# Performance work log

Measured on AMD Instinct MI355X. Metric: run time of the kernel, lower is better.

Reference implementation:

```python
import jax, jax.numpy as jnp
import numpy as np

TOP_K = 2


def setup_inputs() -> dict:
    key = jax.random.key(0)
    k1, k2, k3, k4, k5 = jax.random.split(key, 5)
    B, S, H, F, E = 4, 2048, 1024, 4096, 8
    scale = 1.0 / np.sqrt(H)
    return {
        "hidden_states": jax.random.normal(k1, (B, S, H), dtype=jnp.float32),
        "gate_w": jax.random.normal(k2, (E, H), dtype=jnp.float32) * scale,
        "w1": jax.random.normal(k3, (E, F, H), dtype=jnp.float32) * scale,
        "w3": jax.random.normal(k4, (E, F, H), dtype=jnp.float32) * scale,
        "w2": jax.random.normal(k5, (E, H, F), dtype=jnp.float32) * (1.0 / np.sqrt(F)),
    }


def reference(hidden_states, gate_w, w1, w3, w2):
    B, S, H = hidden_states.shape
    E = gate_w.shape[0]
    x = hidden_states.reshape(-1, H)                    # [T, H], T = B*S

    router_logits = x @ gate_w.T                        # [T, E]
    probs = jax.nn.softmax(router_logits.astype(jnp.float32), axis=-1)
    top_w, top_i = jax.lax.top_k(probs, TOP_K)          # [T, k]
    top_w = top_w / jnp.sum(top_w, axis=-1, keepdims=True)
    top_w = top_w.astype(x.dtype)

    # combine weight of each expert for each token: [E, T]
    one_hot = jax.nn.one_hot(top_i, E, dtype=x.dtype)   # [T, k, E]
    comb = jnp.einsum("tke,tk->et", one_hot, top_w)

    # loop over experts via scan; tokens not routed to expert e have comb==0,
    # which matches the gather/FFN/scatter-combine of the original exactly.
    def body(acc, wts):
        w1e, w3e, w2e, ce = wts
        h = jax.nn.silu(x @ w1e.T) * (x @ w3e.T)        # [T, F]
        return acc + (h @ w2e.T) * ce[:, None], None

    out0 = jnp.zeros_like(x)
    out, _ = jax.lax.scan(body, out0, (w1, w3, w2, comb))
    return out.reshape(B, S, H), router_logits
```

## Files before the change

kernel.cpp:

```cpp
#include <hip/hip_runtime.h>
#include <hip/hip_bf16.h>

#define T_TOK 8192
#define HDIM  1024
#define FDIM  4096
#define NEXP  8

typedef __attribute__((ext_vector_type(8))) short short8;
typedef __attribute__((ext_vector_type(4))) float f32x4;
typedef unsigned short u16;
typedef unsigned int   u32;

#define XB_OFF    0ull
#define W1B_OFF   (XB_OFF   + 16777216ull)
#define W3B_OFF   (W1B_OFF  + 67108864ull)
#define W2B_OFF   (W3B_OFF  + 67108864ull)
#define HBUF_OFF  (W2B_OFF  + 67108864ull)
#define CNT_OFF   (HBUF_OFF + 134217728ull)
#define HOFF_OFF  (CNT_OFF  + 64ull)
#define TLIST_OFF (HOFF_OFF + 64ull)
#define WLIST_OFF (TLIST_OFF + 262144ull)
#define WS_NEED   (WLIST_OFF + 262144ull)

__device__ __forceinline__ u16 f2bf(float f) {
  u32 u = __float_as_uint(f);
  return (u16)((u + 0x7fffu + ((u >> 16) & 1u)) >> 16);
}

__device__ __forceinline__ void gl_lds16(const void* g, void* l) {
  __builtin_amdgcn_global_load_lds(
      (const __attribute__((address_space(1))) void*)g,
      (__attribute__((address_space(3))) void*)l, 16, 0, 0);
}

__global__ __launch_bounds__(256) void prep_kernel(
    const float* __restrict__ x, const float* __restrict__ gw,
    const float* __restrict__ s0, const float* __restrict__ s1, const float* __restrict__ s2,
    u16* __restrict__ d0, u16* __restrict__ d1, u16* __restrict__ d2,
    float* __restrict__ logits, u16* __restrict__ xb,
    int* __restrict__ counts, int* __restrict__ tlist, float* __restrict__ wlist) {
  if (blockIdx.x < 8192) {
    const int n8 = NEXP * FDIM * HDIM / 8;
    const int total = 3 * n8;
    const int stride = 8192 * 256;
    for (int i = blockIdx.x * 256 + threadIdx.x; i < total; i += stride) {
      int seg = i >> 22;
      int j = i & (n8 - 1);
      const float* s = seg == 0 ? s0 : (seg == 1 ? s1 : s2);
      u16* d = seg == 0 ? d0 : (seg == 1 ? d1 : d2);
      float4 v0 = ((const float4*)s)[j * 2];
      float4 v1 = ((const float4*)s)[j * 2 + 1];
      uint4 o;
      o.x = (u32)f2bf(v0.x) | ((u32)f2bf(v0.y) << 16);
      o.y = (u32)f2bf(v0.z) | ((u32)f2bf(v0.w) << 16);
      o.z = (u32)f2bf(v1.x) | ((u32)f2bf(v1.y) << 16);
      o.w = (u32)f2bf(v1.z) | ((u32)f2bf(v1.w) << 16);
      ((uint4*)d)[j] = o;
    }
    return;
  }
  const int wid = threadIdx.x >> 6, lane = threadIdx.x & 63;
  const int t = (blockIdx.x - 8192) * 4 + wid;
  const float* xr = x + (size_t)t * HDIM + lane * 16;
  float4 xv[4];
#pragma unroll
  for (int q = 0; q < 4; ++q) xv[q] = ((const float4*)xr)[q];

  u32 pk[8];
#pragma unroll
  for (int q = 0; q < 4; ++q) {
    pk[q * 2 + 0] = (u32)f2bf(xv[q].x) | ((u32)f2bf(xv[q].y) << 16);
    pk[q * 2 + 1] = (u32)f2bf(xv[q].z) | ((u32)f2bf(xv[q].w) << 16);
  }
  u32* xbo = (u32*)(xb + (size_t)t * HDIM + lane * 16);
  ((uint4*)xbo)[0] = make_uint4(pk[0], pk[1], pk[2], pk[3]);
  ((uint4*)xbo)[1] = make_uint4(pk[4], pk[5], pk[6], pk[7]);

  float lg[NEXP];
#pragma unroll
  for (int e = 0; e < NEXP; ++e) {
    const float4* g = (const float4*)(gw + (size_t)e * HDIM + lane * 16);
    float s = 0.f;
#pragma unroll
    for (int q = 0; q < 4; ++q) {
      float4 gv = g[q];
      s += xv[q].x * gv.x + xv[q].y * gv.y + xv[q].z * gv.z + xv[q].w * gv.w;
    }
#pragma unroll
    for (int off = 32; off > 0; off >>= 1) s += __shfl_xor(s, off, 64);
    lg[e] = s;
  }
  if (lane == 0) {
    float* lo = logits + (size_t)t * NEXP;
#pragma unroll
    for (int e = 0; e < NEXP; ++e) lo[e] = lg[e];
    float v1 = -1e30f, v2 = -1e30f; int i1 = 0, i2 = 0;
#pragma unroll
    for (int e = 0; e < NEXP; ++e) {
      float le = lg[e];
      if (le > v1)      { v2 = v1; i2 = i1; v1 = le; i1 = e; }
      else if (le > v2) { v2 = le; i2 = e; }
    }
    float t2 = __expf(v2 - v1);
    float rs = 1.f / (1.f + t2);
    int p1 = atomicAdd(&counts[i1], 1);
    tlist[i1 * T_TOK + p1] = t; wlist[i1 * T_TOK + p1] = rs;
    int p2 = atomicAdd(&counts[i2], 1);
    tlist[i2 * T_TOK + p2] = t; wlist[i2 * T_TOK + p2] = t2 * rs;
  }
}

__global__ void prefix_kernel(const int* __restrict__ counts, int* __restrict__ hoff) {
  if (threadIdx.x == 0) {
    int s = 0;
    for (int e = 0; e < NEXP; ++e) { hoff[e] = s; s += counts[e]; }
    hoff[NEXP] = s;
  }
}

__global__ __launch_bounds__(512, 2) void ffn1_kernel(
    const u16* __restrict__ xb, const u16* __restrict__ w1b, const u16* __restrict__ w3b,
    u16* __restrict__ hbuf, const int* __restrict__ counts, const int* __restrict__ hoff,
    const int* __restrict__ tlist) {
  const int bid = blockIdx.x;
  const int e  = bid & 7;
  const int j  = bid >> 3;
  const int ct = j >> 6;
  const int rt = j & 63;
  const int Ne = counts[e];
  if (rt * 128 >= Ne) return;

  __shared__ u16 LDS[24576];

  const int tid = threadIdx.x;
  const int wid = tid >> 6, lane = tid & 63;
  const int wr = wid >> 2, wc = wid & 3;
  const int lr = lane & 15, lhi = lane >> 4;

  size_t aoff[2], b1off[2], b3off[2];
#pragma unroll
  for (int q = 0; q < 2; ++q) {
    int idx = q * 512 + tid;
    int r = idx >> 3, c = idx & 7;
    int sw = (c ^ (r & 7)) * 8;
    int grow = rt * 128 + r;
    int gi = grow < Ne ? grow : Ne - 1;
    aoff[q]  = (size_t)tlist[e * T_TOK + gi] * HDIM + sw;
    int fr = ct * 128 + r;
    b1off[q] = ((size_t)e * FDIM + fr) * HDIM + sw;
    b3off[q] = b1off[q];
  }
  const int dW = wid * 512;

  f32x4 acc1[4][2] = {}, acc3[4][2] = {};

  for (int k0 = 0; k0 < HDIM; k0 += 64) {
    __syncthreads();
#pragma unroll
    for (int q = 0; q < 2; ++q) {
      gl_lds16(xb  + aoff[q]  + k0, LDS + q * 4096 + dW);
      gl_lds16(w1b + b1off[q] + k0, LDS + 8192 + q * 4096 + dW);
      gl_lds16(w3b + b3off[q] + k0, LDS + 16384 + q * 4096 + dW);
    }
    __syncthreads();
#pragma unroll
    for (int kk = 0; kk < 2; ++kk) {
      const int chn = ((kk * 4 + lhi) ^ (lr & 7)) * 8;
      short8 af[4], b1f[2], b3f[2];
#pragma unroll
      for (int m = 0; m < 4; ++m)
        af[m] = *(const short8*)(LDS + (wr * 64 + m * 16 + lr) * 64 + chn);
#pragma unroll
      for (int n = 0; n < 2; ++n) {
        int ro = (wc * 32 + n * 16 + lr) * 64 + chn;
        b1f[n] = *(const short8*)(LDS + 8192 + ro);
        b3f[n] = *(const short8*)(LDS + 16384 + ro);
      }
#pragma unroll
      for (int m = 0; m < 4; ++m)
#pragma unroll
        for (int n = 0; n < 2; ++n) {
          acc1[m][n] = __builtin_amdgcn_mfma_f32_16x16x32_bf16(af[m], b1f[n], acc1[m][n], 0, 0, 0);
          acc3[m][n] = __builtin_amdgcn_mfma_f32_16x16x32_bf16(af[m], b3f[n], acc3[m][n], 0, 0, 0);
        }
    }
  }

  const int hb = hoff[e];
  const int rbase = rt * 128 + wr * 64 + lhi * 4;
  const int cbase = ct * 128 + wc * 32 + lr;
#pragma unroll
  for (int m = 0; m < 4; ++m)
#pragma unroll
    for (int i = 0; i < 4; ++i) {
      int grow = rbase + m * 16 + i;
      if (grow < Ne) {
        size_t rowp = (size_t)(hb + grow) * FDIM + cbase;
#pragma unroll
        for (int n = 0; n < 2; ++n) {
          float a1 = acc1[m][n][i], a3 = acc3[m][n][i];
          hbuf[rowp + n * 16] = f2bf((a1 / (1.f + __expf(-a1))) * a3);
        }
      }
    }
}

__global__ __launch_bounds__(256, 2) void ffn2_kernel(
    const u16* __restrict__ hbuf, const u16* __restrict__ w2b,
    float* __restrict__ out, const int* __restrict__ counts, const int* __restrict__ hoff,
    const int* __restrict__ tlist, const float* __restrict__ wlist) {
  const int bid = blockIdx.x;
  const int e  = bid & 7;
  const int j  = bid >> 3;
  const int ct = j >> 6;
  const int rt = j & 63;
  const int Ne = counts[e];
  if (rt * 128 >= Ne) return;
  const int hb = hoff[e];

  __shared__ u16 Alds[128 * 64];
  __shared__ u16 Blds[128 * 64];

  const int tid = threadIdx.x;
  const int wid = tid >> 6, lane = tid & 63;
  const int wr = wid >> 1, wc = wid & 1;
  const int lr = lane & 15, lhi = lane >> 4;

  size_t aoff[4], boff[4]; int ldso[4];
#pragma unroll
  for (int q = 0; q < 4; ++q) {
    int i = wid * 4 + q;
    int r = i * 8 + (lane >> 3);
    int sw = ((lane & 7) ^ (r & 7)) * 8;
    int grow = rt * 128 + r;
    int gi = grow < Ne ? grow : Ne - 1;
    aoff[q] = (size_t)(hb + gi) * FDIM + sw;
    int hr = ct * 128 + r;
    boff[q] = ((size_t)e * HDIM + hr) * FDIM + sw;
    ldso[q] = i * 512;
  }

  f32x4 acc[4][4] = {};

  for (int k0 = 0; k0 < FDIM; k0 += 64) {
    __syncthreads();
#pragma unroll
    for (int q = 0; q < 4; ++q) {
      gl_lds16(hbuf + aoff[q] + k0, Alds + ldso[q]);
      gl_lds16(w2b + boff[q] + k0, Blds + ldso[q]);
    }
    __syncthreads();
#pragma unroll
    for (int kk = 0; kk < 2; ++kk) {
      const int swo = ((kk * 4 + lhi) ^ (lr & 7)) * 8;
      short8 af[4], bf_[4];
#pragma unroll
      for (int m = 0; m < 4; ++m)
        af[m] = *(const short8*)(Alds + (wr * 64 + m * 16 + lr) * 64 + swo);
#pragma unroll
      for (int n = 0; n < 4; ++n)
        bf_[n] = *(const short8*)(Blds + (wc * 64 + n * 16 + lr) * 64 + swo);
#pragma unroll
      for (int m = 0; m < 4; ++m)
#pragma unroll
        for (int n = 0; n < 4; ++n)
          acc[m][n] = __builtin_amdgcn_mfma_f32_16x16x32_bf16(af[m], bf_[n], acc[m][n], 0, 0, 0);
    }
  }

  const int rb = rt * 128 + wr * 64 + lhi * 4;
  const int cb = ct * 128 + wc * 64 + lr;
#pragma unroll
  for (int m = 0; m < 4; ++m)
#pragma unroll
    for (int i = 0; i < 4; ++i) {
      int grow = rb + m * 16 + i;
      if (grow < Ne) {
        int tok = tlist[e * T_TOK + grow];
        float wt = wlist[e * T_TOK + grow];
        float* op = out + (size_t)tok * HDIM + cb;
#pragma unroll
        for (int n = 0; n < 4; ++n)
          atomicAdd(op + n * 16, wt * acc[m][n][i]);
      }
    }
}

extern "C" void kernel_launch(void* const* d_in, const int* in_sizes, int n_in,
                              void* d_out, int out_size, void* d_ws, size_t ws_size,
                              hipStream_t stream) {
  (void)in_sizes; (void)n_in; (void)out_size;
  if (ws_size < WS_NEED) return;

  const float* x  = (const float*)d_in[0];
  const float* gw = (const float*)d_in[1];
  const float* w1 = (const float*)d_in[2];
  const float* w3 = (const float*)d_in[3];
  const float* w2 = (const float*)d_in[4];
  float* out = (float*)d_out;
  float* logits = out + (size_t)T_TOK * HDIM;

  char* ws = (char*)d_ws;
  u16* xb    = (u16*)(ws + XB_OFF);
  u16* w1b   = (u16*)(ws + W1B_OFF);
  u16* w3b   = (u16*)(ws + W3B_OFF);
  u16* w2b   = (u16*)(ws + W2B_OFF);
  u16* hbuf  = (u16*)(ws + HBUF_OFF);
  int* counts = (int*)(ws + CNT_OFF);
  int* hoffp  = (int*)(ws + HOFF_OFF);
  int* tlist  = (int*)(ws + TLIST_OFF);
  float* wlist = (float*)(ws + WLIST_OFF);

  hipMemsetAsync(d_out, 0, (size_t)T_TOK * HDIM * sizeof(float), stream);
  hipMemsetAsync(counts, 0, NEXP * sizeof(int), stream);

  prep_kernel<<<8192 + 2048, 256, 0, stream>>>(x, gw, w1, w3, w2, w1b, w3b, w2b,
                                               logits, xb, counts, tlist, wlist);
  prefix_kernel<<<1, 64, 0, stream>>>(counts, hoffp);
  ffn1_kernel<<<NEXP * 64 * 32, 512, 0, stream>>>(xb, w1b, w3b, hbuf, counts, hoffp, tlist);
  ffn2_kernel<<<NEXP * 64 * 8, 256, 0, stream>>>(hbuf, w2b, out, counts, hoffp, tlist, wlist);
}
```

Measured before the change: 833.2 us.

## Overlap w2 bf16 conversion with ffn1 and shrink FFN tiles for occupancy

Moves the fp32-to-bf16 conversion of w2 out of the prep kernel into extra leading blocks of the ffn1 launch, so the conversion can overlap with the ffn1 GEMM work. Both FFN kernels switch to 256-thread blocks with 128x64 output tiles, less LDS and launch bounds of 4 blocks per CU, which doubles the grid size to raise occupancy. The cost is less data reuse per tile, more global loads of activations, and the conversion blocks competing for bandwidth with the GEMM blocks.

```diff
diff --git a/kernel.cpp b/kernel.cpp
--- a/kernel.cpp
+++ b/kernel.cpp
@@ -5,6 +5,7 @@
 #define HDIM  1024
 #define FDIM  4096
 #define NEXP  8
+#define CVT_BLKS 2048
 
 typedef __attribute__((ext_vector_type(8))) short short8;
 typedef __attribute__((ext_vector_type(4))) float f32x4;
@@ -35,19 +36,19 @@
 
 __global__ __launch_bounds__(256) void prep_kernel(
     const float* __restrict__ x, const float* __restrict__ gw,
-    const float* __restrict__ s0, const float* __restrict__ s1, const float* __restrict__ s2,
-    u16* __restrict__ d0, u16* __restrict__ d1, u16* __restrict__ d2,
+    const float* __restrict__ s0, const float* __restrict__ s1,
+    u16* __restrict__ d0, u16* __restrict__ d1,
     float* __restrict__ logits, u16* __restrict__ xb,
     int* __restrict__ counts, int* __restrict__ tlist, float* __restrict__ wlist) {
   if (blockIdx.x < 8192) {
     const int n8 = NEXP * FDIM * HDIM / 8;
-    const int total = 3 * n8;
+    const int total = 2 * n8;
     const int stride = 8192 * 256;
     for (int i = blockIdx.x * 256 + threadIdx.x; i < total; i += stride) {
       int seg = i >> 22;
       int j = i & (n8 - 1);
-      const float* s = seg == 0 ? s0 : (seg == 1 ? s1 : s2);
-      u16* d = seg == 0 ? d0 : (seg == 1 ? d1 : d2);
+      const float* s = seg == 0 ? s0 : s1;
+      u16* d = seg == 0 ? d0 : d1;
       float4 v0 = ((const float4*)s)[j * 2];
       float4 v1 = ((const float4*)s)[j * 2 + 1];
       uint4 o;
@@ -118,11 +119,27 @@
   }
 }
 
-__global__ __launch_bounds__(512, 2) void ffn1_kernel(
+__global__ __launch_bounds__(256, 4) void ffn1_kernel(
     const u16* __restrict__ xb, const u16* __restrict__ w1b, const u16* __restrict__ w3b,
     u16* __restrict__ hbuf, const int* __restrict__ counts, const int* __restrict__ hoff,
-    const int* __restrict__ tlist) {
-  const int bid = blockIdx.x;
+    const int* __restrict__ tlist,
+    const float* __restrict__ w2src, u16* __restrict__ w2b) {
+  if (blockIdx.x < CVT_BLKS) {
+    const int n8 = NEXP * HDIM * FDIM / 8;
+    const int stride = CVT_BLKS * 256;
+    for (int j = blockIdx.x * 256 + threadIdx.x; j < n8; j += stride) {
+      float4 v0 = ((const float4*)w2src)[j * 2];
+      float4 v1 = ((const float4*)w2src)[j * 2 + 1];
+      uint4 o;
+      o.x = (u32)f2bf(v0.x) | ((u32)f2bf(v0.y) << 16);
+      o.y = (u32)f2bf(v0.z) | ((u32)f2bf(v0.w) << 16);
+      o.z = (u32)f2bf(v1.x) | ((u32)f2bf(v1.y) << 16);
+      o.w = (u32)f2bf(v1.z) | ((u32)f2bf(v1.w) << 16);
+      ((uint4*)w2b)[j] = o;
+    }
+    return;
+  }
+  const int bid = blockIdx.x - CVT_BLKS;
   const int e  = bid & 7;
   const int j  = bid >> 3;
   const int ct = j >> 6;
@@ -130,37 +147,42 @@
   const int Ne = counts[e];
   if (rt * 128 >= Ne) return;
 
-  __shared__ u16 LDS[24576];
+  __shared__ u16 LDS[16384];
 
   const int tid = threadIdx.x;
   const int wid = tid >> 6, lane = tid & 63;
-  const int wr = wid >> 2, wc = wid & 3;
+  const int wr = wid >> 1, wc = wid & 1;
   const int lr = lane & 15, lhi = lane >> 4;
 
-  size_t aoff[2], b1off[2], b3off[2];
-#pragma unroll
-  for (int q = 0; q < 2; ++q) {
-    int idx = q * 512 + tid;
+  size_t aoff[4];
+#pragma unroll
+  for (int q = 0; q < 4; ++q) {
+    int idx = q * 256 + tid;
     int r = idx >> 3, c = idx & 7;
-    int sw = (c ^ (r & 7)) * 8;
     int grow = rt * 128 + r;
     int gi = grow < Ne ? grow : Ne - 1;
-    aoff[q]  = (size_t)tlist[e * T_TOK + gi] * HDIM + sw;
-    int fr = ct * 128 + r;
-    b1off[q] = ((size_t)e * FDIM + fr) * HDIM + sw;
-    b3off[q] = b1off[q];
-  }
-  const int dW = wid * 512;
+    aoff[q] = (size_t)tlist[e * T_TOK + gi] * HDIM + (size_t)((c ^ (r & 7)) * 8);
+  }
+  size_t boff[2];
+#pragma unroll
+  for (int q = 0; q < 2; ++q) {
+    int idx = q * 256 + tid;
+    int r = idx >> 3, c = idx & 7;
+    boff[q] = ((size_t)e * FDIM + ct * 64 + r) * HDIM + (size_t)((c ^ (r & 7)) * 8);
+  }
+  const int dW = wid * 64 * 8;
 
   f32x4 acc1[4][2] = {}, acc3[4][2] = {};
 
   for (int k0 = 0; k0 < HDIM; k0 += 64) {
     __syncthreads();
 #pragma unroll
+    for (int q = 0; q < 4; ++q)
+      gl_lds16(xb + aoff[q] + k0, LDS + q * 2048 + dW);
+#pragma unroll
     for (int q = 0; q < 2; ++q) {
-      gl_lds16(xb  + aoff[q]  + k0, LDS + q * 4096 + dW);
-      gl_lds16(w1b + b1off[q] + k0, LDS + 8192 + q * 4096 + dW);
-      gl_lds16(w3b + b3off[q] + k0, LDS + 16384 + q * 4096 + dW);
+      gl_lds16(w1b + boff[q] + k0, LDS + 8192 + q * 2048 + dW);
+      gl_lds16(w3b + boff[q] + k0, LDS + 12288 + q * 2048 + dW);
     }
     __syncthreads();
 #pragma unroll
@@ -174,7 +196,7 @@
       for (int n = 0; n < 2; ++n) {
         int ro = (wc * 32 + n * 16 + lr) * 64 + chn;
         b1f[n] = *(const short8*)(LDS + 8192 + ro);
-        b3f[n] = *(const short8*)(LDS + 16384 + ro);
+        b3f[n] = *(const short8*)(LDS + 12288 + ro);
       }
 #pragma unroll
       for (int m = 0; m < 4; ++m)
@@ -188,7 +210,7 @@
 
   const int hb = hoff[e];
   const int rbase = rt * 128 + wr * 64 + lhi * 4;
-  const int cbase = ct * 128 + wc * 32 + lr;
+  const int cbase = ct * 64 + wc * 32 + lr;
 #pragma unroll
   for (int m = 0; m < 4; ++m)
 #pragma unroll
@@ -205,7 +227,7 @@
     }
 }
 
-__global__ __launch_bounds__(256, 2) void ffn2_kernel(
+__global__ __launch_bounds__(256, 4) void ffn2_kernel(
     const u16* __restrict__ hbuf, const u16* __restrict__ w2b,
     float* __restrict__ out, const int* __restrict__ counts, const int* __restrict__ hoff,
     const int* __restrict__ tlist, const float* __restrict__ wlist) {
@@ -218,58 +240,62 @@
   if (rt * 128 >= Ne) return;
   const int hb = hoff[e];
 
-  __shared__ u16 Alds[128 * 64];
-  __shared__ u16 Blds[128 * 64];
+  __shared__ u16 LDS[12288];
 
   const int tid = threadIdx.x;
   const int wid = tid >> 6, lane = tid & 63;
   const int wr = wid >> 1, wc = wid & 1;
   const int lr = lane & 15, lhi = lane >> 4;
 
-  size_t aoff[4], boff[4]; int ldso[4];
+  size_t aoff[4];
 #pragma unroll
   for (int q = 0; q < 4; ++q) {
-    int i = wid * 4 + q;
-    int r = i * 8 + (lane >> 3);
-    int sw = ((lane & 7) ^ (r & 7)) * 8;
+    int idx = q * 256 + tid;
+    int r = idx >> 3, c = idx & 7;
     int grow = rt * 128 + r;
     int gi = grow < Ne ? grow : Ne - 1;
-    aoff[q] = (size_t)(hb + gi) * FDIM + sw;
-    int hr = ct * 128 + r;
-    boff[q] = ((size_t)e * HDIM + hr) * FDIM + sw;
-    ldso[q] = i * 512;
-  }
-
-  f32x4 acc[4][4] = {};
+    aoff[q] = (size_t)(hb + gi) * FDIM + (size_t)((c ^ (r & 7)) * 8);
+  }
+  size_t boff[2];
+#pragma unroll
+  for (int q = 0; q < 2; ++q) {
+    int idx = q * 256 + tid;
+    int r = idx >> 3, c = idx & 7;
+    boff[q] = ((size_t)e * HDIM + ct * 64 + r) * FDIM + (size_t)((c ^ (r & 7)) * 8);
+  }
+  const int dW = wid * 64 * 8;
+
+  f32x4 acc[4][2] = {};
 
   for (int k0 = 0; k0 < FDIM; k0 += 64) {
     __syncthreads();
 #pragma unroll
-    for (int q = 0; q < 4; ++q) {
-      gl_lds16(hbuf + aoff[q] + k0, Alds + ldso[q]);
-      gl_lds16(w2b + boff[q] + k0, Blds + ldso[q]);
-    }
+    for (int q = 0; q < 4; ++q)
+      gl_lds16(hbuf + aoff[q] + k0, LDS + q * 2048 + dW);
+#pragma unroll
+    for (int q = 0; q < 2; ++q)
+      gl_lds16(w2b + boff[q] + k0, LDS + 8192 + q * 2048 + dW);
     __syncthreads();
 #pragma unroll
     for (int kk = 0; kk < 2; ++kk) {
-      const int swo = ((kk * 4 + lhi) ^ (lr & 7)) * 8;
-      short8 af[4], bf_[4];
+      const int chn = ((kk * 4 + lhi) ^ (lr & 7)) * 8;
+      short8 af[4], bf_[2];
 #pragma unroll
       for (int m = 0; m < 4; ++m)
-        af[m] = *(const short8*)(Alds + (wr * 64 + m * 16 + lr) * 64 + swo);
-#pragma unroll
-      for (int n = 0; n < 4; ++n)
-        bf_[n] = *(const short8*)(Blds + (wc * 64 + n * 16 + lr) * 64 + swo);
+        af[m] = *(const short8*)(LDS + (wr * 64 + m * 16 + lr) * 64 + chn);
+#pragma unroll
+      for (int n = 0; n < 2; ++n)
+        bf_[n] = *(const short8*)(LDS + 8192 + (wc * 32 + n * 16 + lr) * 64 + chn);
 #pragma unroll
       for (int m = 0; m < 4; ++m)
 #pragma unroll
-        for (int n = 0; n < 4; ++n)
+        for (int n = 0; n < 2; ++n)
           acc[m][n] = __builtin_amdgcn_mfma_f32_16x16x32_bf16(af[m], bf_[n], acc[m][n], 0, 0, 0);
     }
   }
 
   const int rb = rt * 128 + wr * 64 + lhi * 4;
-  const int cb = ct * 128 + wc * 64 + lr;
+  const int cb = ct * 64 + wc * 32 + lr;
 #pragma unroll
   for (int m = 0; m < 4; ++m)
 #pragma unroll
@@ -280,7 +306,7 @@
         float wt = wlist[e * T_TOK + grow];
         float* op = out + (size_t)tok * HDIM + cb;
 #pragma unroll
-        for (int n = 0; n < 4; ++n)
+        for (int n = 0; n < 2; ++n)
           atomicAdd(op + n * 16, wt * acc[m][n][i]);
       }
     }
@@ -314,9 +340,10 @@
   hipMemsetAsync(d_out, 0, (size_t)T_TOK * HDIM * sizeof(float), stream);
   hipMemsetAsync(counts, 0, NEXP * sizeof(int), stream);
 
-  prep_kernel<<<8192 + 2048, 256, 0, stream>>>(x, gw, w1, w3, w2, w1b, w3b, w2b,
+  prep_kernel<<<8192 + 2048, 256, 0, stream>>>(x, gw, w1, w3, w1b, w3b,
                                                logits, xb, counts, tlist, wlist);
   prefix_kernel<<<1, 64, 0, stream>>>(counts, hoffp);
-  ffn1_kernel<<<NEXP * 64 * 32, 512, 0, stream>>>(xb, w1b, w3b, hbuf, counts, hoffp, tlist);
-  ffn2_kernel<<<NEXP * 64 * 8, 256, 0, stream>>>(hbuf, w2b, out, counts, hoffp, tlist, wlist);
-}
+  ffn1_kernel<<<CVT_BLKS + NEXP * 64 * 64, 256, 0, stream>>>(
+      xb, w1b, w3b, hbuf, counts, hoffp, tlist, w2, w2b);
+  ffn2_kernel<<<NEXP * 64 * 16, 256, 0, stream>>>(hbuf, w2b, out, counts, hoffp, tlist, wlist);
+}
```

Result: no change. 832.7 us (-0.1%).
